# Performance work log

Measured on AMD Instinct MI355X. Metric: run time of the kernel, lower is better.

## Reference

```python
import jax, jax.numpy as jnp
import numpy as np

T, D, F, E, TOPK = 4096, 2048, 4096, 8, 2


def setup_inputs() -> dict:
    key = jax.random.key(0)
    ks = jax.random.split(key, 5)
    scale = 0.02
    return {
        "x": jax.random.normal(ks[0], (T, D), dtype=jnp.float32),
        "gate_w": jax.random.normal(ks[1], (D, E), dtype=jnp.float32) * scale,
        "w1": jax.random.normal(ks[2], (E, D, F), dtype=jnp.float32) * scale,
        "w3": jax.random.normal(ks[3], (E, D, F), dtype=jnp.float32) * scale,
        "w2": jax.random.normal(ks[4], (E, F, D), dtype=jnp.float32) * scale,
    }


def reference(x, gate_w, w1, w3, w2):
    # --- top-k gating (matches torch.topk + softmax over selected logits) ---
    gate_logits = x @ gate_w                                   # [T, E]
    top_w, sel = jax.lax.top_k(gate_logits, TOPK)              # [T, K]
    top_w = jax.nn.softmax(top_w.astype(jnp.float32), axis=1).astype(x.dtype)
    # combine weights scattered to dense [T, E]; 0 for unselected experts
    t_idx = jnp.arange(x.shape[0])[:, None]                    # [T, 1]
    cw = jnp.zeros(gate_logits.shape, x.dtype).at[t_idx, sel].add(top_w)  # [T, E]

    # --- all experts as batched GEMMs (SwiGLU FFN), combined by gate weights ---
    h = jnp.einsum('td,edf->etf', x, w1)                       # [E, T, F]
    g = jnp.einsum('td,edf->etf', x, w3)                       # [E, T, F]
    expert_out = jnp.einsum('etf,efd->etd', jax.nn.silu(h) * g, w2)  # [E, T, D]
    return jnp.einsum('te,etd->td', cw, expert_out)            # [T, D]
```

## Files before the change

### kernel.cpp

```cpp
#include <hip/hip_runtime.h>
#include <hip/hip_bf16.h>

#define T_TOK 4096
#define DDIM  2048
#define FDIM  4096
#define NEXP  8
#define MAXROWS 9216
#define MAXMT   72

typedef __attribute__((ext_vector_type(4))) float f32x4;
typedef __attribute__((ext_vector_type(8))) short bf16x8;

__device__ __forceinline__ unsigned short f2b(float f) {
  union { float f; unsigned u; } c; c.f = f;
  unsigned r = c.u + 0x7FFFu + ((c.u >> 16) & 1u);
  return (unsigned short)(r >> 16);
}

__device__ __forceinline__ void gload_lds16(const void* g, void* l) {
  __builtin_amdgcn_global_load_lds((__attribute__((address_space(1))) void*)(g),
                                   (__attribute__((address_space(3))) void*)(l),
                                   16, 0, 0);
}

__device__ __forceinline__ void xcd_map2d(int bid, int MT_PER, int NT, int& mt, int& nt) {
  const int xcd = bid & 7;
  const int li = bid >> 3;
  const int grp = MT_PER * 4;
  const int ng = li / grp;
  const int rem = li % grp;
  mt = xcd * MT_PER + (rem >> 2);
  nt = ng * 4 + (rem & 3);
}

__global__ void gate_topk(const float* __restrict__ x, const float* __restrict__ gw,
                          int* __restrict__ sel_e, float* __restrict__ sel_w) {
  const int t = blockIdx.x * 4 + (threadIdx.x >> 6);
  const int l = threadIdx.x & 63;
  const float* xr = x + (size_t)t * DDIM;
  float acc[8];
  #pragma unroll
  for (int e = 0; e < 8; ++e) acc[e] = 0.f;
  for (int d = l; d < DDIM; d += 64) {
    const float xv = xr[d];
    const float* g = gw + d * 8;
    #pragma unroll
    for (int e = 0; e < 8; ++e) acc[e] = fmaf(xv, g[e], acc[e]);
  }
  #pragma unroll
  for (int e = 0; e < 8; ++e) {
    float v = acc[e];
    #pragma unroll
    for (int off = 32; off; off >>= 1) v += __shfl_xor(v, off, 64);
    acc[e] = v;
  }
  if (l == 0) {
    int e0 = 0; float v0 = acc[0];
    #pragma unroll
    for (int e = 1; e < 8; ++e) if (acc[e] > v0) { v0 = acc[e]; e0 = e; }
    int e1 = -1; float v1 = -1e30f;
    #pragma unroll
    for (int e = 0; e < 8; ++e) if (e != e0 && acc[e] > v1) { v1 = acc[e]; e1 = e; }
    const float ex = __expf(v1 - v0);
    const float w0 = 1.f / (1.f + ex);
    sel_e[t * 2] = e0; sel_e[t * 2 + 1] = e1;
    sel_w[t * 2] = w0; sel_w[t * 2 + 1] = ex * w0;
  }
}

__global__ void build_lists(const int* __restrict__ sel_e, const float* __restrict__ sel_w,
                            int* __restrict__ cnt, int* __restrict__ base,
                            int* __restrict__ row_token, float* __restrict__ row_gw,
                            int* __restrict__ trow) {
  __shared__ int c[8], f[8], b[9];
  const int tid = threadIdx.x;
  if (tid < 8) { c[tid] = 0; f[tid] = 0; }
  __syncthreads();
  for (int t = tid; t < T_TOK; t += 256) {
    atomicAdd(&c[sel_e[t * 2]], 1);
    atomicAdd(&c[sel_e[t * 2 + 1]], 1);
  }
  __syncthreads();
  if (tid == 0) {
    int r = 0;
    for (int e = 0; e < 8; ++e) { b[e] = r; r += ((c[e] + 127) >> 7) << 7; }
    b[8] = r;
    for (int e = 0; e < 8; ++e) { cnt[e] = c[e]; base[e] = b[e]; }
    base[8] = r;
  }
  __syncthreads();
  for (int i = tid; i < MAXROWS; i += 256) { row_token[i] = -1; row_gw[i] = 0.f; }
  __syncthreads();
  for (int t = tid; t < T_TOK; t += 256) {
    #pragma unroll
    for (int k = 0; k < 2; ++k) {
      const int e = sel_e[t * 2 + k];
      const int p = b[e] + atomicAdd(&f[e], 1);
      row_token[p] = t; row_gw[p] = sel_w[t * 2 + k];
      trow[t * 2 + k] = p;
    }
  }
}

__global__ void gather_x(const float* __restrict__ x, const int* __restrict__ base,
                         const int* __restrict__ row_token, unsigned short* __restrict__ xc) {
  const int i = blockIdx.x;
  if (i >= base[8]) return;
  const int t = row_token[i];
  const int tid = threadIdx.x;
  union { uint4 u; unsigned short s[8]; } o;
  if (t < 0) { o.u.x = 0u; o.u.y = 0u; o.u.z = 0u; o.u.w = 0u; }
  else {
    const float4* src = (const float4*)(x + (size_t)t * DDIM + tid * 8);
    const float4 a = src[0], bb = src[1];
    o.s[0] = f2b(a.x);  o.s[1] = f2b(a.y);  o.s[2] = f2b(a.z);  o.s[3] = f2b(a.w);
    o.s[4] = f2b(bb.x); o.s[5] = f2b(bb.y); o.s[6] = f2b(bb.z); o.s[7] = f2b(bb.w);
  }
  ((uint4*)(xc + (size_t)i * DDIM))[tid] = o.u;
}

__device__ __forceinline__ void conv_tile(const float* s, unsigned short* d,
                                          int R, int C, int rowMul, int rowAdd,
                                          int r0, int c0, int tid) {
  __shared__ unsigned short T[64][68];
  {
    const int i = tid >> 2, jb = (tid & 3) * 16;
    #pragma unroll
    for (int k2 = 0; k2 < 4; ++k2) {
      const float4 v = *(const float4*)(s + (size_t)(r0 + i) * C + c0 + jb + k2 * 4);
      uint2 uu;
      uu.x = (unsigned)f2b(v.x) | ((unsigned)f2b(v.y) << 16);
      uu.y = (unsigned)f2b(v.z) | ((unsigned)f2b(v.w) << 16);
      *(uint2*)&T[i][jb + k2 * 4] = uu;
    }
  }
  __syncthreads();
  {
    const int j = tid >> 2, ib = (tid & 3) * 16;
    union { uint4 q[2]; unsigned short s16[16]; } pk;
    #pragma unroll
    for (int i = 0; i < 16; ++i) pk.s16[i] = T[ib + i][j];
    unsigned short* drow = d + (size_t)(rowMul * (c0 + j) + rowAdd) * R + r0 + ib;
    *(uint4*)drow = pk.q[0];
    *(uint4*)(drow + 8) = pk.q[1];
  }
}

__global__ void conv_w13(const float* __restrict__ w1, const float* __restrict__ w3,
                         unsigned short* __restrict__ dst) {
  const int z = blockIdx.z;
  const int e = z & 7;
  const int isw3 = z >> 3;
  const float* s = (isw3 ? w3 : w1) + (size_t)e * DDIM * FDIM;
  unsigned short* d = dst + (size_t)e * DDIM * FDIM * 2;
  conv_tile(s, d, DDIM, FDIM, 2, isw3, blockIdx.x * 64, blockIdx.y * 64, threadIdx.x);
}

__global__ void conv_w2(const float* __restrict__ w2, unsigned short* __restrict__ dst) {
  const int e = blockIdx.z;
  const float* s = w2 + (size_t)e * FDIM * DDIM;
  unsigned short* d = dst + (size_t)e * FDIM * DDIM;
  conv_tile(s, d, FDIM, DDIM, 1, 0, blockIdx.x * 64, blockIdx.y * 64, threadIdx.x);
}

__global__ void moe_gemm1(const unsigned short* __restrict__ A,
                          const unsigned short* __restrict__ B,
                          const int* __restrict__ base,
                          unsigned short* __restrict__ hid) {
  constexpr int KDIM = DDIM;
  constexpr int NDIM = 2 * FDIM;

  int mt, nt;
  xcd_map2d(blockIdx.x, MAXMT / 8, NDIM / 128, mt, nt);

  const int m0 = mt * 128;
  if (m0 >= base[8]) return;
  int e = 0;
  #pragma unroll
  for (int qq = 1; qq < 8; ++qq) if (m0 >= base[qq]) e = qq;
  const int n0 = nt * 128;
  const unsigned short* Bp = B + (size_t)e * NDIM * KDIM;

  __shared__ __align__(16) unsigned short As[128 * 64];
  __shared__ __align__(16) unsigned short Bs[128 * 64];

  const int tid = threadIdx.x;
  const int l = tid & 63;
  const int w = tid >> 6;
  const int wm = w >> 1, wn = w & 1;
  const int lr = l & 15, kc = l >> 4;

  const f32x4 vzero = {0.f, 0.f, 0.f, 0.f};
  f32x4 acc[4][4];
  #pragma unroll
  for (int i = 0; i < 4; ++i)
    #pragma unroll
    for (int j = 0; j < 4; ++j) acc[i][j] = vzero;

  const int srow = w * 32 + (l >> 3);
  const int sc = l & 7;
  const unsigned short* Arow = A + (size_t)(m0 + srow) * KDIM;
  const unsigned short* Brow = Bp + (size_t)(n0 + srow) * KDIM;

  for (int k0 = 0; k0 < KDIM; k0 += 64) {
    #pragma unroll
    for (int qq = 0; qq < 4; ++qq) {
      const int r = srow + qq * 8;
      const int cg = (sc ^ (r & 7)) << 3;
      gload_lds16(Arow + (size_t)qq * 8 * KDIM + k0 + cg,
                  (unsigned short*)As + w * 2048 + qq * 512);
      gload_lds16(Brow + (size_t)qq * 8 * KDIM + k0 + cg,
                  (unsigned short*)Bs + w * 2048 + qq * 512);
    }
    __syncthreads();
    #pragma unroll
    for (int ks = 0; ks < 2; ++ks) {
      bf16x8 af[4], bfr[4];
      #pragma unroll
      for (int mf = 0; mf < 4; ++mf) {
        const int r = wm * 64 + mf * 16 + lr;
        const int c = (ks * 4 + kc) ^ (r & 7);
        af[mf] = *(const bf16x8*)((const char*)As + r * 128 + c * 16);
      }
      #pragma unroll
      for (int nf = 0; nf < 4; ++nf) {
        const int n = wn * 64 + nf * 16 + lr;
        const int c = (ks * 4 + kc) ^ (n & 7);
        bfr[nf] = *(const bf16x8*)((const char*)Bs + n * 128 + c * 16);
      }
      #pragma unroll
      for (int mf = 0; mf < 4; ++mf)
        #pragma unroll
        for (int nf = 0; nf < 4; ++nf)
          acc[mf][nf] = __builtin_amdgcn_mfma_f32_16x16x32_bf16(af[mf], bfr[nf], acc[mf][nf], 0, 0, 0);
    }
    __syncthreads();
  }

  const int fbase = (n0 >> 1) + wn * 32;
  #pragma unroll
  for (int mf = 0; mf < 4; ++mf) {
    const int row = m0 + wm * 64 + mf * 16 + (kc << 2);
    #pragma unroll
    for (int nf = 0; nf < 4; ++nf)
      #pragma unroll
      for (int rr = 0; rr < 4; ++rr) {
        const float v = acc[mf][nf][rr];
        const float o = __shfl_xor(v, 1, 64);
        const float h = (l & 1) ? o : v;
        const float g = (l & 1) ? v : o;
        const float res = (h / (1.f + __expf(-h))) * g;
        const float vc = __shfl(res, (l & 48) | ((l & 7) << 1), 64);
        if (lr < 8)
          hid[(size_t)(row + rr) * FDIM + fbase + nf * 8 + (l & 7)] = f2b(vc);
      }
  }
}

__global__ void moe_gemm2(const unsigned short* __restrict__ A,
                          const unsigned short* __restrict__ B,
                          const int* __restrict__ base,
                          unsigned short* __restrict__ eo) {
  constexpr int KDIM = FDIM;
  constexpr int NDIM = DDIM;

  int mt, ntl;
  xcd_map2d(blockIdx.x, MAXMT / 8, NDIM / 128, mt, ntl);

  const int m0 = mt * 128;
  if (m0 >= base[8]) return;
  int e = 0;
  #pragma unroll
  for (int qq = 1; qq < 8; ++qq) if (m0 >= base[qq]) e = qq;
  const int n0 = ntl * 128;
  const unsigned short* Bp = B + (size_t)e * NDIM * KDIM;

  __shared__ __align__(16) unsigned short As[128 * 64];
  __shared__ __align__(16) unsigned short Bs[128 * 64];

  const int tid = threadIdx.x;
  const int l = tid & 63;
  const int w = tid >> 6;
  const int wm = w >> 1, wn = w & 1;
  const int lr = l & 15, kc = l >> 4;

  const f32x4 vzero = {0.f, 0.f, 0.f, 0.f};
  f32x4 acc[4][4];
  #pragma unroll
  for (int i = 0; i < 4; ++i)
    #pragma unroll
    for (int j = 0; j < 4; ++j) acc[i][j] = vzero;

  const int srow = w * 32 + (l >> 3);
  const int sc = l & 7;
  const unsigned short* Arow = A + (size_t)(m0 + srow) * KDIM;
  const unsigned short* Brow = Bp + (size_t)(n0 + srow) * KDIM;

  for (int k0 = 0; k0 < KDIM; k0 += 64) {
    #pragma unroll
    for (int qq = 0; qq < 4; ++qq) {
      const int r = srow + qq * 8;
      const int cg = (sc ^ (r & 7)) << 3;
      gload_lds16(Arow + (size_t)qq * 8 * KDIM + k0 + cg,
                  (unsigned short*)As + w * 2048 + qq * 512);
      gload_lds16(Brow + (size_t)qq * 8 * KDIM + k0 + cg,
                  (unsigned short*)Bs + w * 2048 + qq * 512);
    }
    __syncthreads();
    #pragma unroll
    for (int ks = 0; ks < 2; ++ks) {
      bf16x8 af[4], bfr[4];
      #pragma unroll
      for (int mf = 0; mf < 4; ++mf) {
        const int r = wm * 64 + mf * 16 + lr;
        const int c = (ks * 4 + kc) ^ (r & 7);
        af[mf] = *(const bf16x8*)((const char*)As + r * 128 + c * 16);
      }
      #pragma unroll
      for (int nf = 0; nf < 4; ++nf) {
        const int n = wn * 64 + nf * 16 + lr;
        const int c = (ks * 4 + kc) ^ (n & 7);
        bfr[nf] = *(const bf16x8*)((const char*)Bs + n * 128 + c * 16);
      }
      #pragma unroll
      for (int mf = 0; mf < 4; ++mf)
        #pragma unroll
        for (int nf = 0; nf < 4; ++nf)
          acc[mf][nf] = __builtin_amdgcn_mfma_f32_16x16x32_bf16(af[mf], bfr[nf], acc[mf][nf], 0, 0, 0);
    }
    __syncthreads();
  }
  #pragma unroll
  for (int mf = 0; mf < 4; ++mf) {
    const int row = m0 + wm * 64 + mf * 16 + (kc << 2);
    #pragma unroll
    for (int rr = 0; rr < 4; ++rr) {
      unsigned short* erow = eo + (size_t)(row + rr) * DDIM;
      #pragma unroll
      for (int nf = 0; nf < 4; ++nf) {
        const int col = n0 + wn * 64 + nf * 16 + lr;
        erow[col] = f2b(acc[mf][nf][rr]);
      }
    }
  }
}

__global__ void combine_k(const unsigned short* __restrict__ eo,
                          const int* __restrict__ trow, const float* __restrict__ sel_w,
                          float* __restrict__ out) {
  const int t = blockIdx.x;
  const int r0 = trow[t * 2], r1 = trow[t * 2 + 1];
  const float w0 = sel_w[t * 2], w1 = sel_w[t * 2 + 1];
  const int c = threadIdx.x * 8;
  union { uint4 u; unsigned short s[8]; } a, b;
  a.u = *(const uint4*)(eo + (size_t)r0 * DDIM + c);
  b.u = *(const uint4*)(eo + (size_t)r1 * DDIM + c);
  float o[8];
  #pragma unroll
  for (int j = 0; j < 8; ++j) {
    union { unsigned u; float f; } fa, fb;
    fa.u = (unsigned)a.s[j] << 16;
    fb.u = (unsigned)b.s[j] << 16;
    o[j] = w0 * fa.f + w1 * fb.f;
  }
  float4* dst = (float4*)(out + (size_t)t * DDIM + c);
  dst[0] = make_float4(o[0], o[1], o[2], o[3]);
  dst[1] = make_float4(o[4], o[5], o[6], o[7]);
}

#define OFF_CNT   0u
#define OFF_BASE  64u
#define OFF_SELE  4096u
#define OFF_SELW  36864u
#define OFF_RTOK  69632u
#define OFF_RGW   106496u
#define OFF_TROW  143360u
#define OFF_XC    1048576u
#define OFF_HID   38797312u
#define OFF_WBUF  114294784u

extern "C" void kernel_launch(void* const* d_in, const int* in_sizes, int n_in,
                              void* d_out, int out_size, void* d_ws, size_t ws_size,
                              hipStream_t stream) {
  const float* x  = (const float*)d_in[0];
  const float* gw = (const float*)d_in[1];
  const float* w1 = (const float*)d_in[2];
  const float* w3 = (const float*)d_in[3];
  const float* w2 = (const float*)d_in[4];
  float* out = (float*)d_out;
  char* ws = (char*)d_ws;

  int*   cnt   = (int*)(ws + OFF_CNT);
  int*   base  = (int*)(ws + OFF_BASE);
  int*   sel_e = (int*)(ws + OFF_SELE);
  float* sel_w = (float*)(ws + OFF_SELW);
  int*   rtok  = (int*)(ws + OFF_RTOK);
  float* rgw   = (float*)(ws + OFF_RGW);
  int*   trow  = (int*)(ws + OFF_TROW);
  unsigned short* xc   = (unsigned short*)(ws + OFF_XC);
  unsigned short* hid  = (unsigned short*)(ws + OFF_HID);
  unsigned short* wbuf = (unsigned short*)(ws + OFF_WBUF);
  unsigned short* eo   = xc;

  gate_topk<<<T_TOK / 4, 256, 0, stream>>>(x, gw, sel_e, sel_w);
  build_lists<<<1, 256, 0, stream>>>(sel_e, sel_w, cnt, base, rtok, rgw, trow);
  gather_x<<<MAXROWS, 256, 0, stream>>>(x, base, rtok, xc);
  conv_w13<<<dim3(32, 64, 16), 256, 0, stream>>>(w1, w3, wbuf);
  moe_gemm1<<<MAXMT * 64, 256, 0, stream>>>(xc, wbuf, base, hid);
  conv_w2<<<dim3(64, 32, 8), 256, 0, stream>>>(w2, wbuf);
  moe_gemm2<<<MAXMT * 16, 256, 0, stream>>>(hid, wbuf, base, eo);
  combine_k<<<T_TOK, 256, 0, stream>>>(eo, trow, sel_w, out);
}
```

Measured before the change: 785.8 us.

## Overlap w2 conversion with gemm1 in a fused heterogeneous kernel

Merges the first expert GEMM and the w2 fp32-to-bf16 transpose conversion into one launch. Within each group of 41 blocks, 9 run GEMM1 tiles and 32 run conversion tiles, so the memory-bound conversion overlaps the compute-bound GEMM. The conversion writes to a separate workspace region so it does not clobber the w1/w3 buffer GEMM1 is still reading. This needs a larger workspace and falls back to the old sequence if the workspace is too small. It also interleaves block types, which may perturb the XCD tile mapping and cache locality of GEMM1.

```diff
diff --git a/kernel.cpp b/kernel.cpp
--- a/kernel.cpp
+++ b/kernel.cpp
@@ -7,6 +7,9 @@
 #define NEXP  8
 #define MAXROWS 9216
 #define MAXMT   72
+#define G1_GRID (MAXMT * 64)
+#define CV2_GRID 16384
+#define FUSED_GRID (512 * 41)
 
 typedef __attribute__((ext_vector_type(4))) float f32x4;
 typedef __attribute__((ext_vector_type(8))) short bf16x8;
@@ -121,8 +124,8 @@
 
 __device__ __forceinline__ void conv_tile(const float* s, unsigned short* d,
                                           int R, int C, int rowMul, int rowAdd,
-                                          int r0, int c0, int tid) {
-  __shared__ unsigned short T[64][68];
+                                          int r0, int c0, int tid,
+                                          unsigned short (*T)[68]) {
   {
     const int i = tid >> 2, jb = (tid & 3) * 16;
     #pragma unroll
@@ -148,30 +151,34 @@
 
 __global__ void conv_w13(const float* __restrict__ w1, const float* __restrict__ w3,
                          unsigned short* __restrict__ dst) {
+  __shared__ unsigned short T[64][68];
   const int z = blockIdx.z;
   const int e = z & 7;
   const int isw3 = z >> 3;
   const float* s = (isw3 ? w3 : w1) + (size_t)e * DDIM * FDIM;
   unsigned short* d = dst + (size_t)e * DDIM * FDIM * 2;
-  conv_tile(s, d, DDIM, FDIM, 2, isw3, blockIdx.x * 64, blockIdx.y * 64, threadIdx.x);
+  conv_tile(s, d, DDIM, FDIM, 2, isw3, blockIdx.x * 64, blockIdx.y * 64, threadIdx.x, T);
 }
 
 __global__ void conv_w2(const float* __restrict__ w2, unsigned short* __restrict__ dst) {
+  __shared__ unsigned short T[64][68];
   const int e = blockIdx.z;
   const float* s = w2 + (size_t)e * FDIM * DDIM;
   unsigned short* d = dst + (size_t)e * FDIM * DDIM;
-  conv_tile(s, d, FDIM, DDIM, 1, 0, blockIdx.x * 64, blockIdx.y * 64, threadIdx.x);
-}
-
-__global__ void moe_gemm1(const unsigned short* __restrict__ A,
-                          const unsigned short* __restrict__ B,
-                          const int* __restrict__ base,
-                          unsigned short* __restrict__ hid) {
+  conv_tile(s, d, FDIM, DDIM, 1, 0, blockIdx.x * 64, blockIdx.y * 64, threadIdx.x, T);
+}
+
+__device__ __forceinline__ void gemm1_body(int bid,
+                                           const unsigned short* __restrict__ A,
+                                           const unsigned short* __restrict__ B,
+                                           const int* __restrict__ base,
+                                           unsigned short* __restrict__ hid,
+                                           unsigned short* As, unsigned short* Bs) {
   constexpr int KDIM = DDIM;
   constexpr int NDIM = 2 * FDIM;
 
   int mt, nt;
-  xcd_map2d(blockIdx.x, MAXMT / 8, NDIM / 128, mt, nt);
+  xcd_map2d(bid, MAXMT / 8, NDIM / 128, mt, nt);
 
   const int m0 = mt * 128;
   if (m0 >= base[8]) return;
@@ -180,9 +187,6 @@
   for (int qq = 1; qq < 8; ++qq) if (m0 >= base[qq]) e = qq;
   const int n0 = nt * 128;
   const unsigned short* Bp = B + (size_t)e * NDIM * KDIM;
-
-  __shared__ __align__(16) unsigned short As[128 * 64];
-  __shared__ __align__(16) unsigned short Bs[128 * 64];
 
   const int tid = threadIdx.x;
   const int l = tid & 63;
@@ -207,10 +211,8 @@
     for (int qq = 0; qq < 4; ++qq) {
       const int r = srow + qq * 8;
       const int cg = (sc ^ (r & 7)) << 3;
-      gload_lds16(Arow + (size_t)qq * 8 * KDIM + k0 + cg,
-                  (unsigned short*)As + w * 2048 + qq * 512);
-      gload_lds16(Brow + (size_t)qq * 8 * KDIM + k0 + cg,
-                  (unsigned short*)Bs + w * 2048 + qq * 512);
+      gload_lds16(Arow + (size_t)qq * 8 * KDIM + k0 + cg, As + w * 2048 + qq * 512);
+      gload_lds16(Brow + (size_t)qq * 8 * KDIM + k0 + cg, Bs + w * 2048 + qq * 512);
     }
     __syncthreads();
     #pragma unroll
@@ -254,6 +256,38 @@
         if (lr < 8)
           hid[(size_t)(row + rr) * FDIM + fbase + nf * 8 + (l & 7)] = f2b(vc);
       }
+  }
+}
+
+__global__ void moe_gemm1(const unsigned short* __restrict__ A,
+                          const unsigned short* __restrict__ B,
+                          const int* __restrict__ base,
+                          unsigned short* __restrict__ hid) {
+  __shared__ __align__(16) unsigned short As[128 * 64];
+  __shared__ __align__(16) unsigned short Bs[128 * 64];
+  gemm1_body(blockIdx.x, A, B, base, hid, As, Bs);
+}
+
+__global__ void gemm1_fused(const unsigned short* __restrict__ A,
+                            const unsigned short* __restrict__ B,
+                            const int* __restrict__ base,
+                            unsigned short* __restrict__ hid,
+                            const float* __restrict__ w2,
+                            unsigned short* __restrict__ w2t) {
+  __shared__ __align__(16) unsigned short As[128 * 64];
+  __shared__ __align__(16) unsigned short Bs[128 * 64];
+  const int g = blockIdx.x / 41;
+  const int r = blockIdx.x % 41;
+  if (r < 9) {
+    gemm1_body(g * 9 + r, A, B, base, hid, As, Bs);
+  } else {
+    const int cid = g * 32 + (r - 9);
+    const int e = cid >> 11;
+    const int rem = cid & 2047;
+    const int r0 = (rem >> 5) * 64;
+    const int c0 = (rem & 31) * 64;
+    conv_tile(w2 + (size_t)e * FDIM * DDIM, w2t + (size_t)e * FDIM * DDIM,
+              FDIM, DDIM, 1, 0, r0, c0, threadIdx.x, (unsigned short (*)[68])As);
   }
 }
 
@@ -378,6 +412,8 @@
 #define OFF_XC    1048576u
 #define OFF_HID   38797312u
 #define OFF_WBUF  114294784u
+#define OFF_W2T   382730240ull
+#define WS_NEED   516947968ull
 
 extern "C" void kernel_launch(void* const* d_in, const int* in_sizes, int n_in,
                               void* d_out, int out_size, void* d_ws, size_t ws_size,
@@ -400,14 +436,23 @@
   unsigned short* xc   = (unsigned short*)(ws + OFF_XC);
   unsigned short* hid  = (unsigned short*)(ws + OFF_HID);
   unsigned short* wbuf = (unsigned short*)(ws + OFF_WBUF);
+  unsigned short* w2t  = (unsigned short*)(ws + OFF_W2T);
   unsigned short* eo   = xc;
+
+  const bool fused = (ws_size >= WS_NEED);
 
   gate_topk<<<T_TOK / 4, 256, 0, stream>>>(x, gw, sel_e, sel_w);
   build_lists<<<1, 256, 0, stream>>>(sel_e, sel_w, cnt, base, rtok, rgw, trow);
   gather_x<<<MAXROWS, 256, 0, stream>>>(x, base, rtok, xc);
   conv_w13<<<dim3(32, 64, 16), 256, 0, stream>>>(w1, w3, wbuf);
-  moe_gemm1<<<MAXMT * 64, 256, 0, stream>>>(xc, wbuf, base, hid);
-  conv_w2<<<dim3(64, 32, 8), 256, 0, stream>>>(w2, wbuf);
-  moe_gemm2<<<MAXMT * 16, 256, 0, stream>>>(hid, wbuf, base, eo);
+
+  if (fused) {
+    gemm1_fused<<<FUSED_GRID, 256, 0, stream>>>(xc, wbuf, base, hid, w2, w2t);
+    moe_gemm2<<<MAXMT * 16, 256, 0, stream>>>(hid, w2t, base, eo);
+  } else {
+    moe_gemm1<<<G1_GRID, 256, 0, stream>>>(xc, wbuf, base, hid);
+    conv_w2<<<dim3(64, 32, 8), 256, 0, stream>>>(w2, wbuf);
+    moe_gemm2<<<MAXMT * 16, 256, 0, stream>>>(hid, wbuf, base, eo);
+  }
   combine_k<<<T_TOK, 256, 0, stream>>>(eo, trow, sel_w, out);
 }
```

Result: no change. 778.0 us (-1.0%).
